# Kernel tuning notes

Measured on AMD Instinct MI355X. Metric: run time of the kernel, lower is better.

## Reference

```python
import jax, jax.numpy as jnp
import numpy as np

L = 16      # number of prior layers backsubstituted through (layer_idx)
D = 1024    # uniform layer width


def setup_inputs() -> dict:
    key = jax.random.key(0)
    ks = jax.random.split(key, 8)
    weights = jax.random.normal(ks[0], (D, D), jnp.float32) / np.sqrt(D)
    biases = jax.random.normal(ks[1], (D, 1), jnp.float32)
    net_x_lowers = jax.random.normal(ks[2], (L, D, D), jnp.float32) / np.sqrt(D)
    net_x_uppers = jax.random.normal(ks[3], (L, D, D), jnp.float32) / np.sqrt(D)
    net_b_lowers = jax.random.normal(ks[4], (L, D, 1), jnp.float32)
    net_b_uppers = jax.random.normal(ks[5], (L, D, 1), jnp.float32)
    input_lowers = jax.random.normal(ks[6], (D, 1), jnp.float32)
    input_uppers = input_lowers + jax.random.uniform(ks[7], (D, 1), jnp.float32)
    return {
        "weights": weights,
        "biases": biases,
        "net_x_lowers": net_x_lowers,
        "net_x_uppers": net_x_uppers,
        "net_b_lowers": net_b_lowers,
        "net_b_uppers": net_b_uppers,
        "input_lowers": input_lowers,
        "input_uppers": input_uppers,
    }


def _backsubstitute(weights, biases, net_x_lowers, net_x_uppers,
                    net_b_lowers, net_b_uppers, input_lowers, input_uppers):
    # Initial relational bounds of the affine layer: y = W^T x + b exactly.
    x0 = weights.T  # (out, in)

    def step(carry, layer):
        xl, xu, bl, bu = carry
        A_lo, A_up, c_lo, c_up = layer
        pl = jnp.maximum(xl, 0.0)
        nl = jnp.minimum(xl, 0.0)
        pu = jnp.maximum(xu, 0.0)
        nu = jnp.minimum(xu, 0.0)
        # intercept accumulation (signed split)
        bl = bl + pl @ c_lo + nl @ c_up
        bu = bu + pu @ c_up + nu @ c_lo
        # coefficient backsubstitution (signed split)
        xl = pl @ A_lo + nl @ A_up
        xu = pu @ A_up + nu @ A_lo
        return (xl, xu, bl, bu), None

    # Loop order: network[layer_idx - i] for i = 0..L-1; the stacked arrays are
    # ordered so index i corresponds to layer (layer_idx - i).
    (xl, xu, bl, bu), _ = jax.lax.scan(
        step,
        (x0, x0, biases, biases),
        (net_x_lowers, net_x_uppers, net_b_lowers, net_b_uppers),
    )

    lo_T = input_lowers.T  # (1, d0)
    up_T = input_uppers.T
    lowers = jnp.sum(jnp.maximum(xl, 0.0) * lo_T + jnp.minimum(xl, 0.0) * up_T,
                     axis=1, keepdims=True) + bl
    uppers = jnp.sum(jnp.maximum(xu, 0.0) * up_T + jnp.minimum(xu, 0.0) * lo_T,
                     axis=1, keepdims=True) + bu
    return jnp.stack([lowers, uppers])  # (2, D, 1)


def reference(weights, biases, net_x_lowers, net_x_uppers,
              net_b_lowers, net_b_uppers, input_lowers, input_uppers):
    return _backsubstitute(weights, biases, net_x_lowers, net_x_uppers,
                           net_b_lowers, net_b_uppers, input_lowers, input_uppers)
```

## Files before the change

### kernel.cpp

```cpp
#include <hip/hip_runtime.h>


#define DD 1024
#define LL 16

typedef _Float16 f16x8 __attribute__((ext_vector_type(8)));
typedef _Float16 f16x4 __attribute__((ext_vector_type(4)));
typedef float f32x4 __attribute__((ext_vector_type(4)));

__device__ __forceinline__ void gload16(const void* gsrc, void* ldst) {
  __builtin_amdgcn_global_load_lds(
      (const __attribute__((address_space(1))) unsigned int*)gsrc,
      (__attribute__((address_space(3))) unsigned int*)ldst, 16, 0, 0);
}

struct GemmTabs {
  const _Float16* xs[2][6];
  const _Float16* as[2][6];
};

__global__ __launch_bounds__(256)
void gemm_step(GemmTabs tabs, float* __restrict__ part)
{
  __shared__ _Float16 smX[2][16][512];
  __shared__ _Float16 smA[2][16][512];

  const int tid  = threadIdx.x;
  const int w    = tid >> 6;
  const int lane = tid & 63;
  const int ln15 = lane & 15;
  const int lhi  = lane >> 4;

  const int lin = blockIdx.x + (blockIdx.y << 3) + (blockIdx.z << 6);
  const int zz  = lin & 7;
  const int j0 = ((lin >> 3) & 7) * 128;
  const int i0 = (lin >> 6) * 128;
  const int lu    = zz >> 2;
  const int split = zz & 3;

  const _Float16* const* xtab = tabs.xs[lu];
  const _Float16* const* atab = tabs.as[lu];

  const int wm = w >> 1, wn = w & 1;

  f32x4 acc[4][4];
#pragma unroll
  for (int a = 0; a < 4; ++a)
#pragma unroll
    for (int b = 0; b < 4; ++b) acc[a][b] = (f32x4){0.f, 0.f, 0.f, 0.f};

  constexpr int NIT = 24;
  const int b_it = (4096 - split * 1536) >> 6;

  auto stage = [&](int buf, int it) {
    const int gk   = split * 1536 + it * 64;
    const int seg  = gk >> 10;
    const int koff = gk & 1023;
    const _Float16* xp = xtab[seg];
    const _Float16* ap = atab[seg];
#pragma unroll
    for (int r = 0; r < 4; ++r) {
      const int f  = r * 4 + w;
      const int rf = f >> 1;
      const int kc = f & 1;
      const int kcol = koff + kc * 32 + lhi * 8;
      gload16(xp + (size_t)(i0 + rf * 16 + ln15) * DD + kcol, &smX[buf][f][0]);
      gload16(ap + (size_t)(j0 + rf * 16 + ln15) * DD + kcol, &smA[buf][f][0]);
    }
  };

  stage(0, 0);

  int buf = 0;
  for (int it = 0; it < NIT; ++it) {
    if (it + 1 < NIT) {
      stage(buf ^ 1, it + 1);
      asm volatile("s_waitcnt vmcnt(8)" ::: "memory");
    } else {
      asm volatile("s_waitcnt vmcnt(0)" ::: "memory");
    }
    __builtin_amdgcn_s_barrier();
    __builtin_amdgcn_sched_barrier(0);

    if (it == b_it) {
#pragma unroll
      for (int a = 0; a < 4; ++a)
#pragma unroll
        for (int b = 0; b < 4; ++b) acc[a][b] *= (1.f / 2048.f);
    }

#pragma unroll
    for (int kc = 0; kc < 2; ++kc) {
      f16x8 xf[4], af[4];
#pragma unroll
      for (int mi = 0; mi < 4; ++mi)
        xf[mi] = *(const f16x8*)&smX[buf][(wm * 4 + mi) * 2 + kc][lane * 8];
#pragma unroll
      for (int ni = 0; ni < 4; ++ni)
        af[ni] = *(const f16x8*)&smA[buf][(wn * 4 + ni) * 2 + kc][lane * 8];
#pragma unroll
      for (int mi = 0; mi < 4; ++mi)
#pragma unroll
        for (int ni = 0; ni < 4; ++ni)
          acc[mi][ni] = __builtin_amdgcn_mfma_f32_16x16x32_f16(xf[mi], af[ni], acc[mi][ni], 0, 0, 0);
    }

    __builtin_amdgcn_sched_barrier(0);
    if (it + 1 < NIT) __builtin_amdgcn_s_barrier();
    buf ^= 1;
  }

  const float eps = (b_it >= NIT) ? (1.f / 2048.f) : 1.f;
  float* outp = part + ((size_t)(split * 2 + lu) << 20);
#pragma unroll
  for (int mi = 0; mi < 4; ++mi) {
    const int r0 = i0 + wm * 64 + mi * 16 + lhi * 4;
#pragma unroll
    for (int ni = 0; ni < 4; ++ni) {
      const int c = j0 + wn * 64 + ni * 16 + ln15;
#pragma unroll
      for (int e = 0; e < 4; ++e)
        outp[(size_t)(r0 + e) * DD + c] = acc[mi][ni][e] * eps;
    }
  }
}

__global__ __launch_bounds__(256)
void convert_prep(int direct,
                  const float* __restrict__ xt, const float* __restrict__ part,
                  const float* __restrict__ cl, const float* __restrict__ cu,
                  _Float16* __restrict__ pl1, _Float16* __restrict__ pl2,
                  _Float16* __restrict__ nl1, _Float16* __restrict__ nl2,
                  _Float16* __restrict__ pu1, _Float16* __restrict__ pu2,
                  _Float16* __restrict__ nu1, _Float16* __restrict__ nu2,
                  float* __restrict__ bl, float* __restrict__ bu,
                  const float* __restrict__ AloN, const float* __restrict__ AupN,
                  _Float16* __restrict__ L1, _Float16* __restrict__ L2,
                  _Float16* __restrict__ U1, _Float16* __restrict__ U2)
{
  __shared__ float shmem[64][68];
  const int t = threadIdx.x;

  if (blockIdx.x < 1024) {
    const int i = blockIdx.x;
    const int k = t * 4;
    const size_t off = (size_t)i * DD + k;

    float Yl[4], Yu[4];
    if (direct) {
      const float4 y = *(const float4*)&xt[off];
      Yl[0] = Yu[0] = y.x; Yl[1] = Yu[1] = y.y; Yl[2] = Yu[2] = y.z; Yl[3] = Yu[3] = y.w;
    } else {
#pragma unroll
      for (int e = 0; e < 4; ++e) { Yl[e] = 0.f; Yu[e] = 0.f; }
#pragma unroll
      for (int s = 0; s < 4; ++s) {
        const float4 a = *(const float4*)&part[((size_t)(s * 2 + 0) << 20) + off];
        const float4 b = *(const float4*)&part[((size_t)(s * 2 + 1) << 20) + off];
        Yl[0] += a.x; Yl[1] += a.y; Yl[2] += a.z; Yl[3] += a.w;
        Yu[0] += b.x; Yu[1] += b.y; Yu[2] += b.z; Yu[3] += b.w;
      }
    }

    const float4 c4l = *(const float4*)&cl[k];
    const float4 c4u = *(const float4*)&cu[k];
    const float Cl[4] = {c4l.x, c4l.y, c4l.z, c4l.w};
    const float Cu[4] = {c4u.x, c4u.y, c4u.z, c4u.w};

    f16x4 o_pl1, o_pl2, o_nl1, o_nl2, o_pu1, o_pu2, o_nu1, o_nu2;
    float blp = 0.f, bup = 0.f;
#pragma unroll
    for (int e = 0; e < 4; ++e) {
      const float pl = fmaxf(Yl[e], 0.f), nl = fminf(Yl[e], 0.f);
      const float pu = fmaxf(Yu[e], 0.f), nu = fminf(Yu[e], 0.f);
      blp += pl * Cl[e] + nl * Cu[e];
      bup += pu * Cu[e] + nu * Cl[e];
      _Float16 h;
      h = (_Float16)pl; o_pl1[e] = h; o_pl2[e] = (_Float16)((pl - (float)h) * 2048.f);
      h = (_Float16)nl; o_nl1[e] = h; o_nl2[e] = (_Float16)((nl - (float)h) * 2048.f);
      h = (_Float16)pu; o_pu1[e] = h; o_pu2[e] = (_Float16)((pu - (float)h) * 2048.f);
      h = (_Float16)nu; o_nu1[e] = h; o_nu2[e] = (_Float16)((nu - (float)h) * 2048.f);
    }
    *(f16x4*)&pl1[off] = o_pl1;  *(f16x4*)&pl2[off] = o_pl2;
    *(f16x4*)&nl1[off] = o_nl1;  *(f16x4*)&nl2[off] = o_nl2;
    *(f16x4*)&pu1[off] = o_pu1;  *(f16x4*)&pu2[off] = o_pu2;
    *(f16x4*)&nu1[off] = o_nu1;  *(f16x4*)&nu2[off] = o_nu2;

#pragma unroll
    for (int o = 32; o > 0; o >>= 1) {
      blp += __shfl_down(blp, o, 64);
      bup += __shfl_down(bup, o, 64);
    }
    if ((t & 63) == 0) { shmem[0][t >> 6] = blp; shmem[1][t >> 6] = bup; }
    __syncthreads();
    if (t == 0) {
      bl[i] += shmem[0][0] + shmem[0][1] + shmem[0][2] + shmem[0][3];
      bu[i] += shmem[1][0] + shmem[1][1] + shmem[1][2] + shmem[1][3];
    }
  } else {
    const int r = blockIdx.x - 1024;
    const int k0 = (r & 15) * 64;
    const int n0 = ((r >> 4) & 15) * 64;
    const int zz = r >> 8;
    const int rid = t >> 4, cid = t & 15;
    const float* src = zz ? AupN : AloN;
    _Float16* d1 = zz ? U1 : L1;
    _Float16* d2 = zz ? U2 : L2;
#pragma unroll
    for (int rr = 0; rr < 4; ++rr) {
      const int kk = rid * 4 + rr;
      *(float4*)&shmem[kk][cid * 4] = *(const float4*)&src[(size_t)(k0 + kk) * DD + n0 + cid * 4];
    }
    __syncthreads();
#pragma unroll
    for (int rr = 0; rr < 4; ++rr) {
      const int n = rid * 4 + rr;
      f16x4 v1, v2;
#pragma unroll
      for (int e = 0; e < 4; ++e) {
        const float v = shmem[cid * 4 + e][n];
        const _Float16 h = (_Float16)v;
        v1[e] = h;
        v2[e] = (_Float16)((v - (float)h) * 2048.f);
      }
      const size_t o = (size_t)(n0 + n) * DD + k0 + cid * 4;
      *(f16x4*)&d1[o] = v1;
      *(f16x4*)&d2[o] = v2;
    }
  }
}

__global__ __launch_bounds__(256)
void transpose_w(const float* __restrict__ W, float* __restrict__ xt)
{
  __shared__ float tile[32][33];
  const int x  = blockIdx.x * 32 + threadIdx.x;
  const int y0 = blockIdx.y * 32 + threadIdx.y;
#pragma unroll
  for (int r = 0; r < 32; r += 8)
    tile[threadIdx.y + r][threadIdx.x] = W[(size_t)(y0 + r) * DD + x];
  __syncthreads();
  const int xo  = blockIdx.y * 32 + threadIdx.x;
  const int yo0 = blockIdx.x * 32 + threadIdx.y;
#pragma unroll
  for (int r = 0; r < 32; r += 8)
    xt[(size_t)(yo0 + r) * DD + xo] = tile[threadIdx.x][threadIdx.y + r];
}

__global__ __launch_bounds__(256)
void bs_final2(const float* __restrict__ part,
               const float* __restrict__ bl, const float* __restrict__ bu,
               const float* __restrict__ inLo, const float* __restrict__ inUp,
               float* __restrict__ out)
{
  const int i = blockIdx.x;
  const int t = threadIdx.x;
  const int k = t * 4;
  const size_t off = (size_t)i * DD + k;
  float Xl[4] = {0.f, 0.f, 0.f, 0.f}, Xu[4] = {0.f, 0.f, 0.f, 0.f};
#pragma unroll
  for (int s = 0; s < 4; ++s) {
    const float4 a = *(const float4*)&part[((size_t)(s * 2 + 0) << 20) + off];
    const float4 b = *(const float4*)&part[((size_t)(s * 2 + 1) << 20) + off];
    Xl[0] += a.x; Xl[1] += a.y; Xl[2] += a.z; Xl[3] += a.w;
    Xu[0] += b.x; Xu[1] += b.y; Xu[2] += b.z; Xu[3] += b.w;
  }
  const float4 lo4 = *(const float4*)&inLo[k];
  const float4 up4 = *(const float4*)&inUp[k];
  const float Lo[4] = {lo4.x, lo4.y, lo4.z, lo4.w};
  const float Up[4] = {up4.x, up4.y, up4.z, up4.w};
  float sl = 0.f, su = 0.f;
#pragma unroll
  for (int e = 0; e < 4; ++e) {
    sl += fmaxf(Xl[e], 0.f) * Lo[e] + fminf(Xl[e], 0.f) * Up[e];
    su += fmaxf(Xu[e], 0.f) * Up[e] + fminf(Xu[e], 0.f) * Lo[e];
  }
#pragma unroll
  for (int o = 32; o > 0; o >>= 1) {
    sl += __shfl_down(sl, o, 64);
    su += __shfl_down(su, o, 64);
  }
  __shared__ float red[2][4];
  if ((t & 63) == 0) { red[0][t >> 6] = sl; red[1][t >> 6] = su; }
  __syncthreads();
  if (t == 0) {
    out[i]      = red[0][0] + red[0][1] + red[0][2] + red[0][3] + bl[i];
    out[DD + i] = red[1][0] + red[1][1] + red[1][2] + red[1][3] + bu[i];
  }
}

#define BM 64
#define BN 64
#define BK 16
#define TM 4
#define TN 4
#define XPAD 4
#define XSTRIDE (BM + XPAD)

struct alignas(16) StepSmem {
  float xl[2][BK][XSTRIDE];
  float xu[2][BK][XSTRIDE];
  float alo[2][BK][BN];
  float aup[2][BK][BN];
  float clo[2][BK];
  float cup[2][BK];
  float bred[8][64];
};

__global__ __launch_bounds__(256)
void bs_step(const float* __restrict__ Xl, const float* __restrict__ Xu,
             float* __restrict__ Yl, float* __restrict__ Yu,
             const float* __restrict__ Alo, const float* __restrict__ Aup,
             const float* __restrict__ Clo, const float* __restrict__ Cup,
             float* __restrict__ bl, float* __restrict__ bu)
{
  __shared__ StepSmem sm;
  const int tid = threadIdx.x;
  const int tx = tid & 15;
  const int ty = tid >> 4;
  const int i0 = blockIdx.y * BM;
  const int j0 = blockIdx.x * BN;
  const bool doBias = (blockIdx.x == 0);
  const int xrow = tid >> 2;
  const int xseg = tid & 3;
  const int arow = tid >> 4;
  const int acol = (tid & 15) * 4;
  const int brow = tid & 63;
  const int bq   = tid >> 6;

  float accl[TM][TN] = {};
  float accu[TM][TN] = {};
  float blp = 0.f, bup = 0.f;
  float4 rxl, rxu, ral, rau;
  float  rc = 0.f;

  auto load_panel = [&](int kp) {
    rxl = *(const float4*)&Xl[(size_t)(i0 + xrow) * DD + kp + xseg * 4];
    rxu = *(const float4*)&Xu[(size_t)(i0 + xrow) * DD + kp + xseg * 4];
    ral = *(const float4*)&Alo[(size_t)(kp + arow) * DD + j0 + acol];
    rau = *(const float4*)&Aup[(size_t)(kp + arow) * DD + j0 + acol];
    if (tid < 32) rc = (tid < 16) ? Clo[kp + tid] : Cup[kp + tid - 16];
  };
  auto store_panel = [&](int b) {
    const float* pxl = (const float*)&rxl;
    const float* pxu = (const float*)&rxu;
#pragma unroll
    for (int s2 = 0; s2 < 4; ++s2) {
      sm.xl[b][xseg * 4 + s2][xrow] = pxl[s2];
      sm.xu[b][xseg * 4 + s2][xrow] = pxu[s2];
    }
    *(float4*)&sm.alo[b][arow][acol] = ral;
    *(float4*)&sm.aup[b][arow][acol] = rau;
    if (tid < 16)      sm.clo[b][tid] = rc;
    else if (tid < 32) sm.cup[b][tid - 16] = rc;
  };

  load_panel(0);
  store_panel(0);
  __syncthreads();

  constexpr int NP = DD / BK;
  for (int p = 0; p < NP; ++p) {
    const int buf = p & 1;
    const bool more = (p + 1 < NP);
    if (more) load_panel((p + 1) * BK);
#pragma unroll 4
    for (int k = 0; k < BK; ++k) {
      const float4 xl4 = *(const float4*)&sm.xl[buf][k][ty * TM];
      const float4 xu4 = *(const float4*)&sm.xu[buf][k][ty * TM];
      const float4 al4 = *(const float4*)&sm.alo[buf][k][tx * TN];
      const float4 au4 = *(const float4*)&sm.aup[buf][k][tx * TN];
      const float xlv[TM] = {xl4.x, xl4.y, xl4.z, xl4.w};
      const float xuv[TM] = {xu4.x, xu4.y, xu4.z, xu4.w};
      const float alv[TN] = {al4.x, al4.y, al4.z, al4.w};
      const float auv[TN] = {au4.x, au4.y, au4.z, au4.w};
#pragma unroll
      for (int m = 0; m < TM; ++m) {
        const float pl = fmaxf(xlv[m], 0.f), nl = fminf(xlv[m], 0.f);
        const float pu = fmaxf(xuv[m], 0.f), nu = fminf(xuv[m], 0.f);
#pragma unroll
        for (int n = 0; n < TN; ++n) {
          accl[m][n] = fmaf(pl, alv[n], fmaf(nl, auv[n], accl[m][n]));
          accu[m][n] = fmaf(pu, auv[n], fmaf(nu, alv[n], accu[m][n]));
        }
      }
    }
    if (doBias) {
#pragma unroll
      for (int kk = 0; kk < 4; ++kk) {
        const int k = bq * 4 + kk;
        const float xlv = sm.xl[buf][k][brow];
        const float xuv = sm.xu[buf][k][brow];
        const float cl = sm.clo[buf][k], cu = sm.cup[buf][k];
        blp += fmaxf(xlv, 0.f) * cl + fminf(xlv, 0.f) * cu;
        bup += fmaxf(xuv, 0.f) * cu + fminf(xuv, 0.f) * cl;
      }
    }
    if (more) store_panel(buf ^ 1);
    __syncthreads();
  }

#pragma unroll
  for (int m = 0; m < TM; ++m) {
    *(float4*)&Yl[(size_t)(i0 + ty * TM + m) * DD + j0 + tx * TN] =
        make_float4(accl[m][0], accl[m][1], accl[m][2], accl[m][3]);
    *(float4*)&Yu[(size_t)(i0 + ty * TM + m) * DD + j0 + tx * TN] =
        make_float4(accu[m][0], accu[m][1], accu[m][2], accu[m][3]);
  }
  if (doBias) {
    sm.bred[bq][brow]     = blp;
    sm.bred[4 + bq][brow] = bup;
    __syncthreads();
    if (tid < 64) {
      const int i = i0 + tid;
      bl[i] += sm.bred[0][tid] + sm.bred[1][tid] + sm.bred[2][tid] + sm.bred[3][tid];
      bu[i] += sm.bred[4][tid] + sm.bred[5][tid] + sm.bred[6][tid] + sm.bred[7][tid];
    }
  }
}

__global__ __launch_bounds__(256)
void bs_transpose_init(const float* __restrict__ W,
                       float* __restrict__ xl, float* __restrict__ xu)
{
  __shared__ float tile[32][33];
  const int x  = blockIdx.x * 32 + threadIdx.x;
  const int y0 = blockIdx.y * 32 + threadIdx.y;
#pragma unroll
  for (int r = 0; r < 32; r += 8)
    tile[threadIdx.y + r][threadIdx.x] = W[(size_t)(y0 + r) * DD + x];
  __syncthreads();
  const int xo  = blockIdx.y * 32 + threadIdx.x;
  const int yo0 = blockIdx.x * 32 + threadIdx.y;
#pragma unroll
  for (int r = 0; r < 32; r += 8) {
    const float v = tile[threadIdx.x][threadIdx.y + r];
    xl[(size_t)(yo0 + r) * DD + xo] = v;
    xu[(size_t)(yo0 + r) * DD + xo] = v;
  }
}

__global__ __launch_bounds__(256)
void bs_final(const float* __restrict__ Xl, const float* __restrict__ Xu,
              const float* __restrict__ bl, const float* __restrict__ bu,
              const float* __restrict__ inLo, const float* __restrict__ inUp,
              float* __restrict__ out)
{
  __shared__ float red[2][4];
  const int i = blockIdx.x;
  const int tid = threadIdx.x;
  const float4 xl4 = *(const float4*)&Xl[(size_t)i * DD + tid * 4];
  const float4 xu4 = *(const float4*)&Xu[(size_t)i * DD + tid * 4];
  const float4 lo4 = *(const float4*)&inLo[tid * 4];
  const float4 up4 = *(const float4*)&inUp[tid * 4];
  const float xlv[4] = {xl4.x, xl4.y, xl4.z, xl4.w};
  const float xuv[4] = {xu4.x, xu4.y, xu4.z, xu4.w};
  const float lov[4] = {lo4.x, lo4.y, lo4.z, lo4.w};
  const float upv[4] = {up4.x, up4.y, up4.z, up4.w};
  float sl = 0.f, su = 0.f;
#pragma unroll
  for (int c = 0; c < 4; ++c) {
    sl += fmaxf(xlv[c], 0.f) * lov[c] + fminf(xlv[c], 0.f) * upv[c];
    su += fmaxf(xuv[c], 0.f) * upv[c] + fminf(xuv[c], 0.f) * lov[c];
  }
#pragma unroll
  for (int off = 32; off > 0; off >>= 1) {
    sl += __shfl_down(sl, off, 64);
    su += __shfl_down(su, off, 64);
  }
  if ((tid & 63) == 0) { red[0][tid >> 6] = sl; red[1][tid >> 6] = su; }
  __syncthreads();
  if (tid == 0) {
    out[i]      = red[0][0] + red[0][1] + red[0][2] + red[0][3] + bl[i];
    out[DD + i] = red[1][0] + red[1][1] + red[1][2] + red[1][3] + bu[i];
  }
}

extern "C" void kernel_launch(void* const* d_in, const int* in_sizes, int n_in,
                              void* d_out, int out_size, void* d_ws, size_t ws_size,
                              hipStream_t stream)
{
  const float* W      = (const float*)d_in[0];
  const float* biases = (const float*)d_in[1];
  const float* AloAll = (const float*)d_in[2];
  const float* AupAll = (const float*)d_in[3];
  const float* CloAll = (const float*)d_in[4];
  const float* CupAll = (const float*)d_in[5];
  const float* inLo   = (const float*)d_in[6];
  const float* inUp   = (const float*)d_in[7];
  float* out = (float*)d_out;

  const size_t NEED = (60ull << 20) + 8192;
  if (ws_size < NEED) {
    float* ws  = (float*)d_ws;
    float* XA  = ws;
    float* XuA = ws + (size_t)DD * DD;
    float* XB  = ws + 2ull * DD * DD;
    float* XuB = ws + 3ull * DD * DD;
    float* bl  = ws + 4ull * DD * DD;
    float* bu  = bl + DD;
    bs_transpose_init<<<dim3(DD / 32, DD / 32), dim3(32, 8), 0, stream>>>(W, XA, XuA);
    hipMemcpyAsync(bl, biases, DD * sizeof(float), hipMemcpyDeviceToDevice, stream);
    hipMemcpyAsync(bu, biases, DD * sizeof(float), hipMemcpyDeviceToDevice, stream);
    const float* xi  = XA;  const float* xui = XuA;
    float*       xo  = XB;  float*       xuo = XuB;
    for (int l = 0; l < LL; ++l) {
      bs_step<<<dim3(DD / BN, DD / BM), 256, 0, stream>>>(
          xi, xui, xo, xuo,
          AloAll + (size_t)l * DD * DD, AupAll + (size_t)l * DD * DD,
          CloAll + (size_t)l * DD,      CupAll + (size_t)l * DD, bl, bu);
      const float* txi = xi; const float* txui = xui;
      xi = xo; xui = xuo;
      xo = (float*)txi; xuo = (float*)txui;
    }
    bs_final<<<DD, 256, 0, stream>>>(xi, xui, bl, bu, inLo, inUp, out);
    return;
  }

  char* ws = (char*)d_ws;
  float*     part = (float*)ws;
  _Float16*  xpl  = (_Float16*)(ws + (32ull << 20));
  _Float16*  apl  = (_Float16*)(ws + (48ull << 20));
  float*     XT   = (float*)(ws + (56ull << 20));
  float*     bl   = (float*)(ws + (60ull << 20));
  float*     bu   = bl + DD;

  auto P = [&](int idx) { return xpl + (size_t)idx * (1u << 20); };
  _Float16 *pl1 = P(0), *pl2 = P(1), *nl1 = P(2), *nl2 = P(3);
  _Float16 *pu1 = P(4), *pu2 = P(5), *nu1 = P(6), *nu2 = P(7);
  _Float16 *AL1 = apl, *AL2 = apl + (1u << 20), *AU1 = apl + (2u << 20), *AU2 = apl + (3u << 20);

  GemmTabs tabs;
  const _Float16* xs0[6] = {pl1, pl2, nl1, nl2, pl1, nl1};
  const _Float16* as0[6] = {AL2, AL1, AU2, AU1, AL1, AU1};
  const _Float16* xs1[6] = {pu1, pu2, nu1, nu2, pu1, nu1};
  const _Float16* as1[6] = {AU2, AU1, AL2, AL1, AU1, AL1};
  for (int s = 0; s < 6; ++s) {
    tabs.xs[0][s] = xs0[s]; tabs.as[0][s] = as0[s];
    tabs.xs[1][s] = xs1[s]; tabs.as[1][s] = as1[s];
  }

  transpose_w<<<dim3(32, 32), dim3(32, 8), 0, stream>>>(W, XT);
  hipMemcpyAsync(bl, biases, DD * sizeof(float), hipMemcpyDeviceToDevice, stream);
  hipMemcpyAsync(bu, biases, DD * sizeof(float), hipMemcpyDeviceToDevice, stream);

  convert_prep<<<1536, 256, 0, stream>>>(1, XT, part, CloAll, CupAll,
                                         pl1, pl2, nl1, nl2, pu1, pu2, nu1, nu2, bl, bu,
                                         AloAll, AupAll, AL1, AL2, AU1, AU2);
  for (int s = 0; s < LL; ++s) {
    gemm_step<<<dim3(8, 8, 8), 256, 0, stream>>>(tabs, part);
    if (s < LL - 1)
      convert_prep<<<1536, 256, 0, stream>>>(0, XT, part,
                                             CloAll + (size_t)(s + 1) * DD,
                                             CupAll + (size_t)(s + 1) * DD,
                                             pl1, pl2, nl1, nl2, pu1, pu2, nu1, nu2, bl, bu,
                                             AloAll + (size_t)(s + 1) * DD * DD,
                                             AupAll + (size_t)(s + 1) * DD * DD,
                                             AL1, AL2, AU1, AU2);
  }
  bs_final2<<<DD, 256, 0, stream>>>(part, bl, bu, inLo, inUp, out);
}
```

Baseline: 1.133 ms.

## Template split-K GEMM on split count and use 6-way split with smaller K tiles

The f16 split-K GEMM is templated on the number of K splits. When the workspace is large enough it now uses 6 splits, launching 768 blocks instead of 512, and stages K in tiles of 32 instead of 64 with half the LDS per block. The workspace layout is compacted so XT reuses the partial-sum buffer, and the reduction kernels sum NS partials. The aim is better CU occupancy and load balance on the GEMM, at the cost of more partial-sum traffic in convert_prep and bs_final2 and more, shorter pipeline iterations.

```diff
diff --git a/kernel.cpp b/kernel.cpp
--- a/kernel.cpp
+++ b/kernel.cpp
@@ -19,11 +19,16 @@
   const _Float16* as[2][6];
 };
 
+template<int NSPLIT>
 __global__ __launch_bounds__(256)
 void gemm_step(GemmTabs tabs, float* __restrict__ part)
 {
-  __shared__ _Float16 smX[2][16][512];
-  __shared__ _Float16 smA[2][16][512];
+  constexpr int KSPL = 6144 / NSPLIT;
+  constexpr int NIT  = KSPL / 32;
+  constexpr int NZ   = 2 * NSPLIT;
+
+  __shared__ _Float16 smX[2][8][512];
+  __shared__ _Float16 smA[2][8][512];
 
   const int tid  = threadIdx.x;
   const int w    = tid >> 6;
@@ -31,41 +36,48 @@
   const int ln15 = lane & 15;
   const int lhi  = lane >> 4;
 
-  const int lin = blockIdx.x + (blockIdx.y << 3) + (blockIdx.z << 6);
-  const int zz  = lin & 7;
-  const int j0 = ((lin >> 3) & 7) * 128;
-  const int i0 = (lin >> 6) * 128;
-  const int lu    = zz >> 2;
-  const int split = zz & 3;
-
-  const _Float16* const* xtab = tabs.xs[lu];
-  const _Float16* const* atab = tabs.as[lu];
+  const int lin = blockIdx.x + gridDim.x * (blockIdx.y + gridDim.y * blockIdx.z);
+  const int zz  = lin % NZ;
+  const int ij  = lin / NZ;
+  const int j0  = (ij & 7) * 128;
+  const int i0  = (ij >> 3) * 128;
+  const int lu    = zz >> (NSPLIT == 6 ? 0 : 0) ? 0 : 0;
+  const int lu_   = zz / NSPLIT;
+  const int split = zz % NSPLIT;
+
+  const _Float16* const* xtab = tabs.xs[lu_];
+  const _Float16* const* atab = tabs.as[lu_];
 
   const int wm = w >> 1, wn = w & 1;
 
+  const int kbase = split * KSPL;
+  const int seg0  = kbase >> 10;
+  const int segB_ = (seg0 + 1 < 6) ? seg0 + 1 : 5;
+  const int it_sw = (((seg0 + 1) << 10) - kbase) >> 5;
+  const _Float16* xpA = xtab[seg0];
+  const _Float16* apA = atab[seg0];
+  const _Float16* xpB = xtab[segB_];
+  const _Float16* apB = atab[segB_];
+
   f32x4 acc[4][4];
 #pragma unroll
   for (int a = 0; a < 4; ++a)
 #pragma unroll
     for (int b = 0; b < 4; ++b) acc[a][b] = (f32x4){0.f, 0.f, 0.f, 0.f};
 
-  constexpr int NIT = 24;
-  const int b_it = (4096 - split * 1536) >> 6;
+  const int b_it = (4096 - kbase) >> 5;
 
   auto stage = [&](int buf, int it) {
-    const int gk   = split * 1536 + it * 64;
-    const int seg  = gk >> 10;
-    const int koff = gk & 1023;
-    const _Float16* xp = xtab[seg];
-    const _Float16* ap = atab[seg];
+    const _Float16* xp = (it < it_sw) ? xpA : xpB;
+    const _Float16* ap = (it < it_sw) ? apA : apB;
+    const int kcol = ((kbase + it * 32) & 1023) + lhi * 8;
 #pragma unroll
     for (int r = 0; r < 4; ++r) {
-      const int f  = r * 4 + w;
-      const int rf = f >> 1;
-      const int kc = f & 1;
-      const int kcol = koff + kc * 32 + lhi * 8;
-      gload16(xp + (size_t)(i0 + rf * 16 + ln15) * DD + kcol, &smX[buf][f][0]);
-      gload16(ap + (size_t)(j0 + rf * 16 + ln15) * DD + kcol, &smA[buf][f][0]);
+      const int f = r * 4 + w;
+      if (f < 8)
+        gload16(xp + (size_t)(i0 + f * 16 + ln15) * DD + kcol, &smX[buf][f & 7][0]);
+      else
+        gload16(ap + (size_t)(j0 + (f - 8) * 16 + ln15) * DD + kcol, &smA[buf][f & 7][0]);
     }
   };
 
@@ -75,7 +87,7 @@
   for (int it = 0; it < NIT; ++it) {
     if (it + 1 < NIT) {
       stage(buf ^ 1, it + 1);
-      asm volatile("s_waitcnt vmcnt(8)" ::: "memory");
+      asm volatile("s_waitcnt vmcnt(4)" ::: "memory");
     } else {
       asm volatile("s_waitcnt vmcnt(0)" ::: "memory");
     }
@@ -89,21 +101,18 @@
         for (int b = 0; b < 4; ++b) acc[a][b] *= (1.f / 2048.f);
     }
 
-#pragma unroll
-    for (int kc = 0; kc < 2; ++kc) {
-      f16x8 xf[4], af[4];
-#pragma unroll
-      for (int mi = 0; mi < 4; ++mi)
-        xf[mi] = *(const f16x8*)&smX[buf][(wm * 4 + mi) * 2 + kc][lane * 8];
+    f16x8 xf[4], af[4];
+#pragma unroll
+    for (int mi = 0; mi < 4; ++mi)
+      xf[mi] = *(const f16x8*)&smX[buf][wm * 4 + mi][lane * 8];
+#pragma unroll
+    for (int ni = 0; ni < 4; ++ni)
+      af[ni] = *(const f16x8*)&smA[buf][wn * 4 + ni][lane * 8];
+#pragma unroll
+    for (int mi = 0; mi < 4; ++mi)
 #pragma unroll
       for (int ni = 0; ni < 4; ++ni)
-        af[ni] = *(const f16x8*)&smA[buf][(wn * 4 + ni) * 2 + kc][lane * 8];
-#pragma unroll
-      for (int mi = 0; mi < 4; ++mi)
-#pragma unroll
-        for (int ni = 0; ni < 4; ++ni)
-          acc[mi][ni] = __builtin_amdgcn_mfma_f32_16x16x32_f16(xf[mi], af[ni], acc[mi][ni], 0, 0, 0);
-    }
+        acc[mi][ni] = __builtin_amdgcn_mfma_f32_16x16x32_f16(xf[mi], af[ni], acc[mi][ni], 0, 0, 0);
 
     __builtin_amdgcn_sched_barrier(0);
     if (it + 1 < NIT) __builtin_amdgcn_s_barrier();
@@ -111,7 +120,7 @@
   }
 
   const float eps = (b_it >= NIT) ? (1.f / 2048.f) : 1.f;
-  float* outp = part + ((size_t)(split * 2 + lu) << 20);
+  float* outp = part + ((size_t)(split * 2 + lu_) << 20);
 #pragma unroll
   for (int mi = 0; mi < 4; ++mi) {
     const int r0 = i0 + wm * 64 + mi * 16 + lhi * 4;
@@ -125,6 +134,7 @@
   }
 }
 
+template<int NS>
 __global__ __launch_bounds__(256)
 void convert_prep(int direct,
                   const float* __restrict__ xt, const float* __restrict__ part,
@@ -154,7 +164,7 @@
 #pragma unroll
       for (int e = 0; e < 4; ++e) { Yl[e] = 0.f; Yu[e] = 0.f; }
 #pragma unroll
-      for (int s = 0; s < 4; ++s) {
+      for (int s = 0; s < NS; ++s) {
         const float4 a = *(const float4*)&part[((size_t)(s * 2 + 0) << 20) + off];
         const float4 b = *(const float4*)&part[((size_t)(s * 2 + 1) << 20) + off];
         Yl[0] += a.x; Yl[1] += a.y; Yl[2] += a.z; Yl[3] += a.w;
@@ -247,6 +257,7 @@
     xt[(size_t)(yo0 + r) * DD + xo] = tile[threadIdx.x][threadIdx.y + r];
 }
 
+template<int NS>
 __global__ __launch_bounds__(256)
 void bs_final2(const float* __restrict__ part,
                const float* __restrict__ bl, const float* __restrict__ bu,
@@ -259,7 +270,7 @@
   const size_t off = (size_t)i * DD + k;
   float Xl[4] = {0.f, 0.f, 0.f, 0.f}, Xu[4] = {0.f, 0.f, 0.f, 0.f};
 #pragma unroll
-  for (int s = 0; s < 4; ++s) {
+  for (int s = 0; s < NS; ++s) {
     const float4 a = *(const float4*)&part[((size_t)(s * 2 + 0) << 20) + off];
     const float4 b = *(const float4*)&part[((size_t)(s * 2 + 1) << 20) + off];
     Xl[0] += a.x; Xl[1] += a.y; Xl[2] += a.z; Xl[3] += a.w;
@@ -476,6 +487,56 @@
   }
 }
 
+template<int NS>
+static void run_f16(const float* W, const float* biases,
+                    const float* AloAll, const float* AupAll,
+                    const float* CloAll, const float* CupAll,
+                    const float* inLo, const float* inUp,
+                    float* out, char* ws, hipStream_t stream)
+{
+  float*     part = (float*)ws;
+  _Float16*  xpl  = (_Float16*)(ws + ((size_t)NS * 8ull << 20));
+  _Float16*  apl  = (_Float16*)(ws + (((size_t)NS * 8ull + 16) << 20));
+  float*     bl   = (float*)(ws + (((size_t)NS * 8ull + 24) << 20));
+  float*     bu   = bl + DD;
+  float*     XT   = part;
+
+  auto P = [&](int idx) { return xpl + (size_t)idx * (1u << 20); };
+  _Float16 *pl1 = P(0), *pl2 = P(1), *nl1 = P(2), *nl2 = P(3);
+  _Float16 *pu1 = P(4), *pu2 = P(5), *nu1 = P(6), *nu2 = P(7);
+  _Float16 *AL1 = apl, *AL2 = apl + (1u << 20), *AU1 = apl + (2u << 20), *AU2 = apl + (3u << 20);
+
+  GemmTabs tabs;
+  const _Float16* xs0[6] = {pl1, pl2, nl1, nl2, pl1, nl1};
+  const _Float16* as0[6] = {AL2, AL1, AU2, AU1, AL1, AU1};
+  const _Float16* xs1[6] = {pu1, pu2, nu1, nu2, pu1, nu1};
+  const _Float16* as1[6] = {AU2, AU1, AL2, AL1, AU1, AL1};
+  for (int s = 0; s < 6; ++s) {
+    tabs.xs[0][s] = xs0[s]; tabs.as[0][s] = as0[s];
+    tabs.xs[1][s] = xs1[s]; tabs.as[1][s] = as1[s];
+  }
+
+  transpose_w<<<dim3(32, 32), dim3(32, 8), 0, stream>>>(W, XT);
+  hipMemcpyAsync(bl, biases, DD * sizeof(float), hipMemcpyDeviceToDevice, stream);
+  hipMemcpyAsync(bu, biases, DD * sizeof(float), hipMemcpyDeviceToDevice, stream);
+
+  convert_prep<NS><<<1536, 256, 0, stream>>>(1, XT, part, CloAll, CupAll,
+                                             pl1, pl2, nl1, nl2, pu1, pu2, nu1, nu2, bl, bu,
+                                             AloAll, AupAll, AL1, AL2, AU1, AU2);
+  for (int s = 0; s < LL; ++s) {
+    gemm_step<NS><<<dim3(8, 8, 2 * NS), 256, 0, stream>>>(tabs, part);
+    if (s < LL - 1)
+      convert_prep<NS><<<1536, 256, 0, stream>>>(0, XT, part,
+                                                 CloAll + (size_t)(s + 1) * DD,
+                                                 CupAll + (size_t)(s + 1) * DD,
+                                                 pl1, pl2, nl1, nl2, pu1, pu2, nu1, nu2, bl, bu,
+                                                 AloAll + (size_t)(s + 1) * DD * DD,
+                                                 AupAll + (size_t)(s + 1) * DD * DD,
+                                                 AL1, AL2, AU1, AU2);
+  }
+  bs_final2<NS><<<DD, 256, 0, stream>>>(part, bl, bu, inLo, inUp, out);
+}
+
 extern "C" void kernel_launch(void* const* d_in, const int* in_sizes, int n_in,
                               void* d_out, int out_size, void* d_ws, size_t ws_size,
                               hipStream_t stream)
@@ -490,73 +551,38 @@
   const float* inUp   = (const float*)d_in[7];
   float* out = (float*)d_out;
 
-  const size_t NEED = (60ull << 20) + 8192;
-  if (ws_size < NEED) {
-    float* ws  = (float*)d_ws;
-    float* XA  = ws;
-    float* XuA = ws + (size_t)DD * DD;
-    float* XB  = ws + 2ull * DD * DD;
-    float* XuB = ws + 3ull * DD * DD;
-    float* bl  = ws + 4ull * DD * DD;
-    float* bu  = bl + DD;
-    bs_transpose_init<<<dim3(DD / 32, DD / 32), dim3(32, 8), 0, stream>>>(W, XA, XuA);
-    hipMemcpyAsync(bl, biases, DD * sizeof(float), hipMemcpyDeviceToDevice, stream);
-    hipMemcpyAsync(bu, biases, DD * sizeof(float), hipMemcpyDeviceToDevice, stream);
-    const float* xi  = XA;  const float* xui = XuA;
-    float*       xo  = XB;  float*       xuo = XuB;
-    for (int l = 0; l < LL; ++l) {
-      bs_step<<<dim3(DD / BN, DD / BM), 256, 0, stream>>>(
-          xi, xui, xo, xuo,
-          AloAll + (size_t)l * DD * DD, AupAll + (size_t)l * DD * DD,
-          CloAll + (size_t)l * DD,      CupAll + (size_t)l * DD, bl, bu);
-      const float* txi = xi; const float* txui = xui;
-      xi = xo; xui = xuo;
-      xo = (float*)txi; xuo = (float*)txui;
-    }
-    bs_final<<<DD, 256, 0, stream>>>(xi, xui, bl, bu, inLo, inUp, out);
+  const size_t NEED6 = (72ull << 20) + 8192;
+  const size_t NEED4 = (56ull << 20) + 8192;
+
+  if (ws_size >= NEED6) {
+    run_f16<6>(W, biases, AloAll, AupAll, CloAll, CupAll, inLo, inUp, out, (char*)d_ws, stream);
     return;
   }
-
-  char* ws = (char*)d_ws;
-  float*     part = (float*)ws;
-  _Float16*  xpl  = (_Float16*)(ws + (32ull << 20));
-  _Float16*  apl  = (_Float16*)(ws + (48ull << 20));
-  float*     XT   = (float*)(ws + (56ull << 20));
-  float*     bl   = (float*)(ws + (60ull << 20));
-  float*     bu   = bl + DD;
-
-  auto P = [&](int idx) { return xpl + (size_t)idx * (1u << 20); };
-  _Float16 *pl1 = P(0), *pl2 = P(1), *nl1 = P(2), *nl2 = P(3);
-  _Float16 *pu1 = P(4), *pu2 = P(5), *nu1 = P(6), *nu2 = P(7);
-  _Float16 *AL1 = apl, *AL2 = apl + (1u << 20), *AU1 = apl + (2u << 20), *AU2 = apl + (3u << 20);
-
-  GemmTabs tabs;
-  const _Float16* xs0[6] = {pl1, pl2, nl1, nl2, pl1, nl1};
-  const _Float16* as0[6] = {AL2, AL1, AU2, AU1, AL1, AU1};
-  const _Float16* xs1[6] = {pu1, pu2, nu1, nu2, pu1, nu1};
-  const _Float16* as1[6] = {AU2, AU1, AL2, AL1, AU1, AL1};
-  for (int s = 0; s < 6; ++s) {
-    tabs.xs[0][s] = xs0[s]; tabs.as[0][s] = as0[s];
-    tabs.xs[1][s] = xs1[s]; tabs.as[1][s] = as1[s];
-  }
-
-  transpose_w<<<dim3(32, 32), dim3(32, 8), 0, stream>>>(W, XT);
+  if (ws_size >= NEED4) {
+    run_f16<4>(W, biases, AloAll, AupAll, CloAll, CupAll, inLo, inUp, out, (char*)d_ws, stream);
+    return;
+  }
+
+  float* ws  = (float*)d_ws;
+  float* XA  = ws;
+  float* XuA = ws + (size_t)DD * DD;
+  float* XB  = ws + 2ull * DD * DD;
+  float* XuB = ws + 3ull * DD * DD;
+  float* bl  = ws + 4ull * DD * DD;
+  float* bu  = bl + DD;
+  bs_transpose_init<<<dim3(DD / 32, DD / 32), dim3(32, 8), 0, stream>>>(W, XA, XuA);
   hipMemcpyAsync(bl, biases, DD * sizeof(float), hipMemcpyDeviceToDevice, stream);
   hipMemcpyAsync(bu, biases, DD * sizeof(float), hipMemcpyDeviceToDevice, stream);
-
-  convert_prep<<<1536, 256, 0, stream>>>(1, XT, part, CloAll, CupAll,
-                                         pl1, pl2, nl1, nl2, pu1, pu2, nu1, nu2, bl, bu,
-                                         AloAll, AupAll, AL1, AL2, AU1, AU2);
-  for (int s = 0; s < LL; ++s) {
-    gemm_step<<<dim3(8, 8, 8), 256, 0, stream>>>(tabs, part);
-    if (s < LL - 1)
-      convert_prep<<<1536, 256, 0, stream>>>(0, XT, part,
-                                             CloAll + (size_t)(s + 1) * DD,
-                                             CupAll + (size_t)(s + 1) * DD,
-                                             pl1, pl2, nl1, nl2, pu1, pu2, nu1, nu2, bl, bu,
-                                             AloAll + (size_t)(s + 1) * DD * DD,
-                                             AupAll + (size_t)(s + 1) * DD * DD,
-                                             AL1, AL2, AU1, AU2);
-  }
-  bs_final2<<<DD, 256, 0, stream>>>(part, bl, bu, inLo, inUp, out);
-}
+  const float* xi  = XA;  const float* xui = XuA;
+  float*       xo  = XB;  float*       xuo = XuB;
+  for (int l = 0; l < LL; ++l) {
+    bs_step<<<dim3(DD / BN, DD / BM), 256, 0, stream>>>(
+        xi, xui, xo, xuo,
+        AloAll + (size_t)l * DD * DD, AupAll + (size_t)l * DD * DD,
+        CloAll + (size_t)l * DD,      CupAll + (size_t)l * DD, bl, bu);
+    const float* txi = xi; const float* txui = xui;
+    xi = xo; xui = xuo;
+    xo = (float*)txi; xuo = (float*)txui;
+  }
+  bs_final<<<DD, 256, 0, stream>>>(xi, xui, bl, bu, inLo, inUp, out);
+}
```

New measurement: 1.210 ms. 1.07x slower.
